# Kernel tuning notes

Hardware: AMD Instinct MI355X
Metric: run time of the kernel (lower is better)

Reference implementation:

```python
import math
import jax, jax.numpy as jnp
import numpy as np

L, F, K = 3, 128, 20          # layers, hidden size, rbf size
CUTOFF = 5.0
B, NPER, EPER = 4, 4096, 49152  # graphs, nodes/graph, edges/graph
NVOC = 119                    # len(ase.data.atomic_numbers)
PNAMES = ['atom_emb','pot_W','pot_b','init_W1','init_b1','init_W2','init_b2','vec_w',
          'filt_W','filt_b','msg_W1','msg_b1','msg_W2','msg_b2','U_W','V_W',
          'upd_W1','upd_b1','upd_W2','upd_b2']


def _painn(atom_xyz, cell, nodes, atom_edges, edges_displacement, V_flat, E_flat, p):
    N = B * NPER
    pos = atom_xyz.reshape(N, 3)
    # edge_offset = cumsum(num_nodes) ; all graphs have NPER nodes
    off = (jnp.arange(B, dtype=atom_edges.dtype) * NPER)[:, None, None]
    edges = (atom_edges + off).reshape(B * EPER, 2)
    # calc_distance with periodic cell offsets
    disp = jnp.einsum('bec,bcd->bed', edges_displacement, cell).reshape(B * EPER, 3)
    send, recv = edges[:, 0], edges[:, 1]
    diff = pos[recv] - (pos[send] + disp)                       # [E,3]
    dist = jnp.sqrt(jnp.sum(diff * diff, axis=1, keepdims=True))  # [E,1]
    # sinc RBF expansion
    n_range = jnp.arange(1, K + 1, dtype=jnp.float32)
    edge_state = jnp.sin(dist * n_range * (math.pi / CUTOFF)) / dist  # [E,K]
    # init scalar features: Embedding(Z) || Linear(V) -> MLP
    s_atom = p['atom_emb'][nodes.reshape(N)]                    # [N,F]
    s_pot = V_flat @ p['pot_W'].T + p['pot_b']                  # [N,F]
    h = jnp.concatenate([s_atom, s_pot], axis=-1)
    s = jax.nn.silu(h @ p['init_W1'].T + p['init_b1']) @ p['init_W2'].T + p['init_b2']  # [N,F]
    # init vector features: no-bias Linear(1->F) on E field
    v = E_flat[:, :, None] * p['vec_w']                         # [N,3,F]
    cut = jnp.where(dist < CUTOFF, 0.5 * (jnp.cos(math.pi * dist / CUTOFF) + 1.0), 0.0)  # [E,1]
    dirn = diff / jnp.maximum(dist, 1e-12)                      # [E,3]
    s_list, v_list = [], []
    for l in range(L):
        # --- PaiNNInteraction ---
        fw = (edge_state @ p['filt_W'][l].T + p['filt_b'][l]) * cut                # [E,3F]
        so = jax.nn.silu(s @ p['msg_W1'][l].T + p['msg_b1'][l]) @ p['msg_W2'][l].T + p['msg_b2'][l]  # [N,3F]
        fo = fw * so[send]                                                          # [E,3F]
        g_sv, g_ev, g_ns = jnp.split(fo, 3, axis=1)
        msg_s = s[send] * g_ns                                                      # [E,F]
        msg_v = v[send] * g_sv[:, None, :] + g_ev[:, None, :] * dirn[:, :, None]    # [E,3,F]
        s = s + jax.ops.segment_sum(msg_s, recv, num_segments=N)
        v = v + jax.ops.segment_sum(msg_v, recv, num_segments=N)
        # --- PaiNNUpdate ---
        Uv = v @ p['U_W'][l].T                                                      # [N,3,F]
        Vv = v @ p['V_W'][l].T                                                      # [N,3,F]
        Vn = jnp.sqrt(jnp.sum(Vv * Vv, axis=1))                                     # [N,F]
        m = jnp.concatenate([s, Vn], axis=1)
        m = jax.nn.silu(m @ p['upd_W1'][l].T + p['upd_b1'][l]) @ p['upd_W2'][l].T + p['upd_b2'][l]
        a_ss, a_sv, a_vv = jnp.split(m, 3, axis=1)
        s = s + a_ss + a_sv * jnp.sum(Uv * Vv, axis=1)
        v = v + a_vv[:, None, :] * Uv
        s_list.append(s)
        v_list.append(v)
    # pack trajectory: [L,N,1,F] scalar || [L,N,3,F] vector -> [L,N,4,F]
    return jnp.concatenate([jnp.stack(s_list)[:, :, None, :], jnp.stack(v_list)], axis=2)


def setup_inputs() -> dict:
    key = jax.random.key(0)
    ks = iter(jax.random.split(key, 48))
    def nrm(shape, scale=0.05):
        return jax.random.normal(next(ks), shape, dtype=jnp.float32) * scale
    atom_xyz = jax.random.uniform(next(ks), (B, NPER, 3), dtype=jnp.float32) * 30.0
    cell = jnp.tile(jnp.eye(3, dtype=jnp.float32)[None] * 30.0, (B, 1, 1))
    nodes = jax.random.randint(next(ks), (B, NPER), 0, NVOC)
    e0 = jax.random.randint(next(ks), (B, EPER), 0, NPER)
    delta = jax.random.randint(next(ks), (B, EPER), 1, NPER)
    e1 = (e0 + delta) % NPER  # sender != receiver -> no zero-distance edges
    atom_edges = jnp.stack([e0, e1], axis=-1)
    edges_displacement = jax.random.randint(next(ks), (B, EPER, 3), -1, 2).astype(jnp.float32)
    V_flat = nrm((B * NPER, 1), 1.0)
    E_flat = nrm((B * NPER, 3), 1.0)
    params = dict(
        atom_emb=nrm((NVOC, F), 1.0),
        pot_W=nrm((F, 1)), pot_b=nrm((F,)),
        init_W1=nrm((F, 2 * F)), init_b1=nrm((F,)),
        init_W2=nrm((F, F)), init_b2=nrm((F,)),
        vec_w=nrm((F,)),
        filt_W=nrm((L, 3 * F, K)), filt_b=nrm((L, 3 * F)),
        msg_W1=nrm((L, F, F)), msg_b1=nrm((L, F)),
        msg_W2=nrm((L, 3 * F, F)), msg_b2=nrm((L, 3 * F)),
        U_W=nrm((L, F, F)), V_W=nrm((L, F, F)),
        upd_W1=nrm((L, F, 2 * F)), upd_b1=nrm((L, F)),
        upd_W2=nrm((L, 3 * F, F)), upd_b2=nrm((L, 3 * F)),
    )
    return dict(atom_xyz=atom_xyz, cell=cell, nodes=nodes, atom_edges=atom_edges,
                edges_displacement=edges_displacement, V_flat=V_flat, E_flat=E_flat, **params)


def reference(atom_xyz, cell, nodes, atom_edges, edges_displacement, V_flat, E_flat,
              atom_emb, pot_W, pot_b, init_W1, init_b1, init_W2, init_b2, vec_w,
              filt_W, filt_b, msg_W1, msg_b1, msg_W2, msg_b2, U_W, V_W,
              upd_W1, upd_b1, upd_W2, upd_b2):
    p = dict(zip(PNAMES, (atom_emb, pot_W, pot_b, init_W1, init_b1, init_W2, init_b2, vec_w,
                          filt_W, filt_b, msg_W1, msg_b1, msg_W2, msg_b2, U_W, V_W,
                          upd_W1, upd_b1, upd_W2, upd_b2)))
    return _painn(atom_xyz, cell, nodes, atom_edges, edges_displacement, V_flat, E_flat, p)
```

## Files before the change

### kernel.cpp

```cpp
#include <hip/hip_runtime.h>
#include <math.h>

#define NPER  4096
#define NTOT  16384
#define EPER  49152
#define ETOT  196608
#define FD    128
#define F3    384
#define KR    20
#define PI_F  3.14159265358979f

typedef unsigned short u16;
typedef __attribute__((ext_vector_type(8))) short s16x8;
typedef __attribute__((ext_vector_type(4))) float f32x4;
typedef _Float16 h16x2 __attribute__((ext_vector_type(2)));
typedef _Float16 h16x4 __attribute__((ext_vector_type(4)));
typedef _Float16 h16x8 __attribute__((ext_vector_type(8)));

#if defined(__has_builtin)
#if __has_builtin(__builtin_amdgcn_fdot2)
#define FDOT2(a,b,c) __builtin_amdgcn_fdot2((a),(b),(c),false)
#endif
#endif
#ifndef FDOT2
#define FDOT2(a,b,c) ((float)(a)[0]*(float)(b)[0] + (float)(a)[1]*(float)(b)[1] + (c))
#endif

__device__ __forceinline__ float silu_f(float x){ return x / (1.0f + __expf(-x)); }
__device__ __forceinline__ u16 f2b(float x){
    unsigned u = __float_as_uint(x);
    u = u + 0x7FFFu + ((u >> 16) & 1u);
    return (u16)(u >> 16);
}
__device__ __forceinline__ float b2f(u16 h){ return __uint_as_float(((unsigned)h) << 16); }

struct __align__(16) EdgeRec {
    float4 ed;
    h16x8  es0;
    h16x8  es1;
    h16x4  es2;
    h16x4  pad;
};

__global__ __launch_bounds__(256) void edge_kernel(
    const float* __restrict__ xyz, const float* __restrict__ cell,
    const int* __restrict__ aedges, const float* __restrict__ edisp,
    int* __restrict__ sendb, int* __restrict__ recvb,
    EdgeRec* __restrict__ erec, int* __restrict__ counts)
{
    int e = blockIdx.x * blockDim.x + threadIdx.x;
    if (e >= ETOT) return;
    int b = e / EPER;
    int s = aedges[(size_t)e*2+0] + b*NPER;
    int r = aedges[(size_t)e*2+1] + b*NPER;
    const float* cb = cell + b*9;
    float c0 = edisp[(size_t)e*3+0], c1 = edisp[(size_t)e*3+1], c2 = edisp[(size_t)e*3+2];
    float diff[3];
    #pragma unroll
    for (int d=0; d<3; ++d) {
        float disp = c0*cb[d] + c1*cb[3+d] + c2*cb[6+d];
        diff[d] = xyz[(size_t)r*3+d] - (xyz[(size_t)s*3+d] + disp);
    }
    float dist = sqrtf(diff[0]*diff[0]+diff[1]*diff[1]+diff[2]*diff[2]);
    float cut = (dist < 5.0f) ? 0.5f*(__cosf(PI_F*dist*0.2f)+1.0f) : 0.0f;
    float invg = 1.0f/fmaxf(dist,1e-12f);
    EdgeRec rec;
    rec.ed = make_float4(diff[0]*invg, diff[1]*invg, diff[2]*invg, cut);
    float theta = dist*(PI_F*0.2f);
    float s1 = __sinf(theta), cth = __cosf(theta);
    float scale = cut / dist;
    float twoc = 2.f*cth;
    float sm1 = 0.f, sk = s1;
    _Float16 esv[20];
    #pragma unroll
    for (int k=0;k<20;++k){
        esv[k] = (_Float16)(sk*scale);
        float nx = twoc*sk - sm1;
        sm1 = sk; sk = nx;
    }
    union { h16x8 v; _Float16 h[8]; } u0, u1;
    union { h16x4 v; _Float16 h[4]; } u2;
    #pragma unroll
    for (int i=0;i<8;++i){ u0.h[i]=esv[i]; u1.h[i]=esv[8+i]; }
    #pragma unroll
    for (int i=0;i<4;++i) u2.h[i]=esv[16+i];
    rec.es0=u0.v; rec.es1=u1.v; rec.es2=u2.v;
    rec.pad = (h16x4)((_Float16)0);
    erec[e] = rec;
    sendb[e]=s; recvb[e]=r;
    atomicAdd(&counts[r],1);
}

__global__ __launch_bounds__(1024) void scan_kernel(const int* __restrict__ counts,
                                                    int* __restrict__ row_off)
{
    __shared__ int sdata[1024];
    int t = threadIdx.x;
    int base = t * 16;
    int local[16];
    int s = 0;
    #pragma unroll
    for (int i=0;i<16;++i){ local[i]=s; s += counts[base+i]; }
    sdata[t] = s;
    __syncthreads();
    for (int off=1; off<1024; off<<=1) {
        int val = (t>=off) ? sdata[t-off] : 0;
        __syncthreads();
        sdata[t] += val;
        __syncthreads();
    }
    int chunk_off = (t==0) ? 0 : sdata[t-1];
    #pragma unroll
    for (int i=0;i<16;++i) row_off[base+i] = chunk_off + local[i];
    if (t==1023) row_off[NTOT] = sdata[1023];
}

__global__ __launch_bounds__(256) void fill_kernel(
    const int* __restrict__ recvb, const int* __restrict__ sendb,
    const EdgeRec* __restrict__ erec,
    const int* __restrict__ row_off, int* __restrict__ cursor,
    int* __restrict__ sd_csr, EdgeRec* __restrict__ erec_csr)
{
    int e = blockIdx.x * blockDim.x + threadIdx.x;
    if (e >= ETOT) return;
    int r = recvb[e];
    int slot = atomicAdd(&cursor[r], 1);
    int pos = row_off[r] + slot;
    sd_csr[pos] = sendb[e];
    erec_csr[pos] = erec[e];
}

__global__ __launch_bounds__(256) void wconv_kernel(
    const float* __restrict__ w0, const float* __restrict__ w1,
    const float* __restrict__ w2, const float* __restrict__ w3,
    const float* __restrict__ w4, const float* __restrict__ w5,
    const float* __restrict__ w6, const float* __restrict__ w7,
    u16* __restrict__ dst)
{
    int t = blockIdx.x*256 + threadIdx.x;
    if (t >= 589824) return;
    const float* src; int off; int d = t;
    if      (t < 32768)  { src=w0; off=t; }
    else if (t < 49152)  { src=w1; off=t-32768; }
    else if (t < 98304)  { src=w2; off=t-49152; }
    else if (t < 245760) { src=w3; off=t-98304; }
    else if (t < 294912) { int o=t-245760; int l=o>>14; int r=o&16383; src=w4; off=o;
                           d = 245760 + l*32768 + r; }
    else if (t < 344064) { int o=t-294912; int l=o>>14; int r=o&16383; src=w5; off=o;
                           d = 245760 + l*32768 + 16384 + r; }
    else if (t < 442368) { src=w6; off=t-344064; }
    else                 { src=w7; off=t-442368; }
    dst[d] = f2b(src[off]);
}

__global__ __launch_bounds__(256) void wfilt_kernel(const float* __restrict__ fW,
                                                    _Float16* __restrict__ dst)
{
    int t = blockIdx.x*256 + threadIdx.x;
    if (t < 3*F3*KR) dst[t] = (_Float16)fW[t];
}

__global__ __launch_bounds__(256) void hbuild_kernel(const int* __restrict__ nodes,
    const float* __restrict__ atom_emb, const float* __restrict__ V_flat,
    const float* __restrict__ pot_W, const float* __restrict__ pot_b,
    u16* __restrict__ h)
{
    int t = blockIdx.x * blockDim.x + threadIdx.x;
    int n = t >> 8, k = t & 255;
    float val;
    if (k < FD) val = atom_emb[(size_t)nodes[n]*FD + k];
    else { int f = k - FD; val = V_flat[n]*pot_W[f] + pot_b[f]; }
    h[t] = f2b(val);
}

__global__ __launch_bounds__(256) void v0_kernel(const float* __restrict__ E_flat,
    const float* __restrict__ vec_w, float* __restrict__ v0, u16* __restrict__ vq)
{
    int t = blockIdx.x * blockDim.x + threadIdx.x;
    int n = t / F3, r = t - n*F3;
    int c = r >> 7, f = r & 127;
    float val = E_flat[(size_t)n*3 + c] * vec_w[f];
    v0[t] = val;
    vq[((size_t)n*FD + f)*4 + c] = f2b(val);
}

template<int ACT>
__global__ __launch_bounds__(256) void bgemm_kernel(
    const u16* __restrict__ A, int lda,
    const u16* __restrict__ W, int Kdim,
    const float* __restrict__ bias,
    float* __restrict__ C, int ldc,
    u16* __restrict__ Cb, int ldcb,
    u16* __restrict__ Cq, int qoff)
{
    const int tid  = threadIdx.x;
    const int wave = tid >> 6, lane = tid & 63;
    const int q = lane >> 4, im = lane & 15;
    const int row0 = blockIdx.y*64 + wave*16;
    const int col0 = blockIdx.x*64;
    f32x4 acc[4];
    #pragma unroll
    for (int n=0;n<4;++n) acc[n] = (f32x4){0.f,0.f,0.f,0.f};
    const u16* Ap = A + (size_t)(row0+im)*lda + q*8;
    const u16* Wp = W + (size_t)(col0+im)*Kdim + q*8;
    for (int k0 = 0; k0 < Kdim; k0 += 32) {
        s16x8 af = *(const s16x8*)(Ap + k0);
        #pragma unroll
        for (int n=0;n<4;++n) {
            s16x8 bf = *(const s16x8*)(Wp + (size_t)n*16*Kdim + k0);
            acc[n] = __builtin_amdgcn_mfma_f32_16x16x32_bf16(af, bf, acc[n], 0, 0, 0);
        }
    }
    #pragma unroll
    for (int n=0;n<4;++n) {
        int col = col0 + n*16 + im;
        float bv = bias ? bias[col] : 0.f;
        #pragma unroll
        for (int r=0;r<4;++r) {
            int row = row0 + q*4 + r;
            float v = acc[n][r] + bv;
            if (ACT) v = silu_f(v);
            if (C)  C[(size_t)row*ldc + col] = v;
            if (Cb) Cb[(size_t)row*ldcb + col] = f2b(v);
            if (Cq) Cq[((size_t)row*FD + (col & 127))*4 + (col >> 7) + qoff] = f2b(v);
        }
    }
}

#define HID_OFF(row, col2b) ((unsigned)((row)*256 + (col2b)*2) ^ ((unsigned)((row)&7) << 4))

__global__ __launch_bounds__(256) void msgmlp_kernel(
    const u16* __restrict__ A,
    const u16* __restrict__ W1,
    const float* __restrict__ b1,
    const u16* __restrict__ W2,
    const float* __restrict__ b2,
    u16* __restrict__ sq)
{
    __shared__ u16 hid[16*FD];
    const int tid = threadIdx.x;
    const int wave = tid >> 6, lane = tid & 63;
    const int q = lane >> 4, im = lane & 15;
    const int row0 = blockIdx.x * 16;
    {
        f32x4 acc[2];
        #pragma unroll
        for (int n=0;n<2;++n) acc[n] = (f32x4){0.f,0.f,0.f,0.f};
        const u16* Ap = A + (size_t)(row0+im)*FD + q*8;
        #pragma unroll
        for (int k0=0;k0<FD;k0+=32) {
            s16x8 af = *(const s16x8*)(Ap + k0);
            #pragma unroll
            for (int n=0;n<2;++n) {
                s16x8 bf = *(const s16x8*)(W1 + (size_t)(wave*32+n*16+im)*FD + k0 + q*8);
                acc[n] = __builtin_amdgcn_mfma_f32_16x16x32_bf16(af, bf, acc[n], 0, 0, 0);
            }
        }
        #pragma unroll
        for (int n=0;n<2;++n) {
            int col = wave*32 + n*16 + im;
            float bv = b1[col];
            #pragma unroll
            for (int r=0;r<4;++r) {
                int row = q*4 + r;
                *(u16*)((char*)hid + HID_OFF(row, col)) = f2b(silu_f(acc[n][r]+bv));
            }
        }
    }
    __syncthreads();
    s16x8 af[4];
    #pragma unroll
    for (int k=0;k<4;++k)
        af[k] = *(const s16x8*)((char*)hid + HID_OFF(im, k*32+q*8));
    #pragma unroll
    for (int jj=0;jj<2;++jj) {
        int j = wave*2 + jj;
        f32x4 a2[3];
        #pragma unroll
        for (int g=0;g<3;++g) a2[g] = (f32x4){0.f,0.f,0.f,0.f};
        #pragma unroll
        for (int k=0;k<4;++k) {
            #pragma unroll
            for (int g=0;g<3;++g) {
                s16x8 bf = *(const s16x8*)(W2 + (size_t)(g*128 + j*16 + im)*FD + k*32 + q*8);
                a2[g] = __builtin_amdgcn_mfma_f32_16x16x32_bf16(af[k], bf, a2[g], 0, 0, 0);
            }
        }
        int fcol = j*16 + im;
        float c0 = b2[fcol], c1 = b2[FD+fcol], c2 = b2[2*FD+fcol];
        #pragma unroll
        for (int r=0;r<4;++r) {
            int row = row0 + q*4 + r;
            size_t t4 = ((size_t)row*FD + fcol)*4;
            unsigned pk = (unsigned)f2b(a2[0][r]+c0) | ((unsigned)f2b(a2[1][r]+c1) << 16);
            *(unsigned*)(sq + t4) = pk;
            sq[t4+2] = f2b(a2[2][r]+c2);
        }
    }
}

__global__ __launch_bounds__(256) void updmlp_kernel(
    const u16* __restrict__ A,
    const u16* __restrict__ W1,
    const float* __restrict__ b1,
    const u16* __restrict__ W2,
    const float* __restrict__ b2,
    const float* __restrict__ s_mid, const float* __restrict__ dotb,
    const float* __restrict__ v_mid, const float* __restrict__ Uv,
    float* __restrict__ outp, u16* __restrict__ s_bf,
    u16* __restrict__ sq, u16* __restrict__ vq)
{
    __shared__ u16 hid[16*FD];
    const int tid = threadIdx.x;
    const int wave = tid >> 6, lane = tid & 63;
    const int q = lane >> 4, im = lane & 15;
    const int row0 = blockIdx.x * 16;
    {
        f32x4 acc[2];
        #pragma unroll
        for (int n=0;n<2;++n) acc[n] = (f32x4){0.f,0.f,0.f,0.f};
        const u16* Ap = A + (size_t)(row0+im)*256 + q*8;
        #pragma unroll
        for (int k0=0;k0<256;k0+=32) {
            s16x8 af = *(const s16x8*)(Ap + k0);
            #pragma unroll
            for (int n=0;n<2;++n) {
                s16x8 bf = *(const s16x8*)(W1 + (size_t)(wave*32+n*16+im)*256 + k0 + q*8);
                acc[n] = __builtin_amdgcn_mfma_f32_16x16x32_bf16(af, bf, acc[n], 0, 0, 0);
            }
        }
        #pragma unroll
        for (int n=0;n<2;++n) {
            int col = wave*32 + n*16 + im;
            float bv = b1[col];
            #pragma unroll
            for (int r=0;r<4;++r) {
                int row = q*4 + r;
                *(u16*)((char*)hid + HID_OFF(row, col)) = f2b(silu_f(acc[n][r]+bv));
            }
        }
    }
    __syncthreads();
    s16x8 af[4];
    #pragma unroll
    for (int k=0;k<4;++k)
        af[k] = *(const s16x8*)((char*)hid + HID_OFF(im, k*32+q*8));
    #pragma unroll
    for (int jj=0;jj<2;++jj) {
        int j = wave*2 + jj;
        f32x4 a2[3];
        #pragma unroll
        for (int g=0;g<3;++g) a2[g] = (f32x4){0.f,0.f,0.f,0.f};
        #pragma unroll
        for (int k=0;k<4;++k) {
            #pragma unroll
            for (int g=0;g<3;++g) {
                s16x8 bf = *(const s16x8*)(W2 + (size_t)(g*128 + j*16 + im)*FD + k*32 + q*8);
                a2[g] = __builtin_amdgcn_mfma_f32_16x16x32_bf16(af[k], bf, a2[g], 0, 0, 0);
            }
        }
        int fcol = j*16 + im;
        float b_ss = b2[fcol], b_sv = b2[FD+fcol], b_vv = b2[2*FD+fcol];
        #pragma unroll
        for (int r=0;r<4;++r) {
            int row = row0 + q*4 + r;
            float a_ss = a2[0][r] + b_ss;
            float a_sv = a2[1][r] + b_sv;
            float a_vv = a2[2][r] + b_vv;
            size_t t = (size_t)row*FD + fcol;
            float sval = s_mid[t] + a_ss + a_sv*dotb[t];
            outp[(size_t)row*512 + fcol] = sval;
            s_bf[t] = f2b(sval);
            sq[t*4 + 3] = f2b(sval);
            ushort4 pack;
            #pragma unroll
            for (int c=0;c<3;++c) {
                size_t vi = ((size_t)row*3 + c)*FD + fcol;
                float vval = v_mid[vi] + a_vv*Uv[((size_t)row*4 + c)*FD + fcol];
                outp[(size_t)row*512 + (1+c)*FD + fcol] = vval;
                ((u16*)&pack)[c] = f2b(vval);
            }
            ((u16*)&pack)[3] = 0;
            *(ushort4*)(vq + t*4) = pack;
        }
    }
}

__global__ __launch_bounds__(256) void uvdot_kernel(
    const u16* __restrict__ A,
    const u16* __restrict__ W,
    float* __restrict__ Uv,
    float* __restrict__ dotb,
    u16* __restrict__ mbuf)
{
    const int tid  = threadIdx.x;
    const int wave = tid >> 6, lane = tid & 63;
    const int q = lane >> 4, im = lane & 15;
    const int row0 = blockIdx.x*64 + wave*16;
    const int node = (row0 >> 2) + q;
    const u16* Ap = A + (size_t)(row0+im)*FD + q*8;
    s16x8 af[4];
    #pragma unroll
    for (int k=0;k<4;++k) af[k] = *(const s16x8*)(Ap + k*32);
    #pragma unroll
    for (int j=0;j<8;++j) {
        f32x4 aU = (f32x4){0.f,0.f,0.f,0.f};
        f32x4 aV = (f32x4){0.f,0.f,0.f,0.f};
        const u16* WpU = W + (size_t)(j*16+im)*FD + q*8;
        const u16* WpV = WpU + (size_t)128*FD;
        #pragma unroll
        for (int k=0;k<4;++k) {
            s16x8 bU = *(const s16x8*)(WpU + k*32);
            s16x8 bV = *(const s16x8*)(WpV + k*32);
            aU = __builtin_amdgcn_mfma_f32_16x16x32_bf16(af[k], bU, aU, 0, 0, 0);
            aV = __builtin_amdgcn_mfma_f32_16x16x32_bf16(af[k], bV, aV, 0, 0, 0);
        }
        int fcol = j*16 + im;
        float u0=aU[0], u1=aU[1], u2=aU[2];
        float w0=aV[0], w1=aV[1], w2=aV[2];
        dotb[(size_t)node*FD + fcol] = u0*w0 + u1*w1 + u2*w2;
        mbuf[(size_t)node*256 + FD + fcol] = f2b(sqrtf(w0*w0 + w1*w1 + w2*w2));
        size_t ub = ((size_t)node*4)*FD + fcol;
        Uv[ub]      = u0;
        Uv[ub+FD]   = u1;
        Uv[ub+2*FD] = u2;
    }
}

__device__ __forceinline__ void edge_step(
    const EdgeRec& er, ushort4 s4, ushort4 v4,
    const h16x2* wp,
    float b0, float b1, float b2,
    float& acc_s, float& av0, float& av1, float& av2)
{
    union { h16x8 v; h16x2 p[4]; } e0, e1;
    union { h16x4 v; h16x2 p[2]; } e2;
    e0.v = er.es0; e1.v = er.es1; e2.v = er.es2;
    h16x2 ep[10] = {e0.p[0],e0.p[1],e0.p[2],e0.p[3],
                    e1.p[0],e1.p[1],e1.p[2],e1.p[3],
                    e2.p[0],e2.p[1]};
    float4 ed = er.ed;
    float d0=0.f, d1=0.f, d2=0.f;
    #pragma unroll
    for (int j=0;j<10;++j){
        d0 = FDOT2(ep[j], wp[j],    d0);
        d1 = FDOT2(ep[j], wp[10+j], d1);
        d2 = FDOT2(ep[j], wp[20+j], d2);
    }
    float g_sv = d0 + b0*ed.w;
    float g_ev = d1 + b1*ed.w;
    float g_ns = d2 + b2*ed.w;
    float fo_sv = g_sv * b2f(s4.x);
    float fo_ev = g_ev * b2f(s4.y);
    float fo_ns = g_ns * b2f(s4.z);
    acc_s += b2f(s4.w) * fo_ns;
    av0 += b2f(v4.x)*fo_sv + fo_ev*ed.x;
    av1 += b2f(v4.y)*fo_sv + fo_ev*ed.y;
    av2 += b2f(v4.z)*fo_sv + fo_ev*ed.z;
}

__global__ __launch_bounds__(256) __attribute__((amdgpu_waves_per_eu(4,8)))
void agg_kernel(
    const float* __restrict__ s_prev_f, int s_ldaf,
    const float* __restrict__ v_prev_f, int v_nstrf,
    const ushort4* __restrict__ sq, const ushort4* __restrict__ vq,
    const EdgeRec* __restrict__ erec_csr,
    const int* __restrict__ sd_csr, const int* __restrict__ row_off,
    const _Float16* __restrict__ wf, const float* __restrict__ fb,
    float* __restrict__ s_mid, float* __restrict__ v_mid,
    u16* __restrict__ vmid4_bf, u16* __restrict__ mbuf)
{
    const int f   = threadIdx.x & 127;
    const int sub = threadIdx.x >> 7;
    h16x2 wp[30];
    #pragma unroll
    for (int rsel=0; rsel<3; ++rsel){
        const h16x4* rp = (const h16x4*)(wf + (size_t)(rsel*FD + f)*KR);
        #pragma unroll
        for (int i=0;i<5;++i){
            union { h16x4 v; h16x2 p[2]; } t; t.v = rp[i];
            wp[rsel*10+2*i]   = t.p[0];
            wp[rsel*10+2*i+1] = t.p[1];
        }
    }
    const float b0 = fb[f], b1 = fb[FD+f], b2 = fb[2*FD+f];

    const int n = blockIdx.x*2 + sub;
    const int beg = __builtin_amdgcn_readfirstlane(row_off[n]);
    const int end = __builtin_amdgcn_readfirstlane(row_off[n+1]);
    float acc_s=0.f, av0=0.f, av1=0.f, av2=0.f;

    int i0 = (beg   < end) ? beg   : 0;
    int i1 = (beg+1 < end) ? beg+1 : i0;
    int sd0 = __builtin_amdgcn_readfirstlane(sd_csr[i0]);
    int sd1 = __builtin_amdgcn_readfirstlane(sd_csr[i1]);
    ushort4 sA = sq[(size_t)sd0*FD + f];
    ushort4 vA = vq[(size_t)sd0*FD + f];
    ushort4 sB = sq[(size_t)sd1*FD + f];
    ushort4 vB = vq[(size_t)sd1*FD + f];
    EdgeRec r0 = erec_csr[i0];
    EdgeRec r1 = erec_csr[i1];

    for (int idx = beg; idx + 2 <= end; idx += 2) {
        int j0 = (idx+2 < end) ? idx+2 : 0;
        int j1 = (idx+3 < end) ? idx+3 : j0;
        int nsd0 = __builtin_amdgcn_readfirstlane(sd_csr[j0]);
        int nsd1 = __builtin_amdgcn_readfirstlane(sd_csr[j1]);
        ushort4 nsA = sq[(size_t)nsd0*FD + f];
        ushort4 nvA = vq[(size_t)nsd0*FD + f];
        ushort4 nsB = sq[(size_t)nsd1*FD + f];
        ushort4 nvB = vq[(size_t)nsd1*FD + f];
        EdgeRec nr0 = erec_csr[j0];
        EdgeRec nr1 = erec_csr[j1];

        edge_step(r0, sA, vA, wp, b0,b1,b2, acc_s, av0, av1, av2);
        edge_step(r1, sB, vB, wp, b0,b1,b2, acc_s, av0, av1, av2);

        sA=nsA; vA=nvA; sB=nsB; vB=nvB; r0=nr0; r1=nr1;
    }
    if (((end - beg) & 1) && beg < end) {
        edge_step(r0, sA, vA, wp, b0,b1,b2, acc_s, av0, av1, av2);
    }

    float smv = s_prev_f[(size_t)n*s_ldaf+f] + acc_s;
    s_mid[(size_t)n*FD+f] = smv;
    mbuf[(size_t)n*256+f] = f2b(smv);
    const float* vp = v_prev_f + (size_t)n*v_nstrf;
    float o0 = vp[f]+av0, o1 = vp[FD+f]+av1, o2 = vp[2*FD+f]+av2;
    size_t vo = (size_t)n*F3;
    v_mid[vo+f]=o0;        v_mid[vo+FD+f]=o1;        v_mid[vo+2*FD+f]=o2;
    size_t v4 = (size_t)n*512;
    vmid4_bf[v4+f]=f2b(o0); vmid4_bf[v4+FD+f]=f2b(o1); vmid4_bf[v4+2*FD+f]=f2b(o2);
}

extern "C" void kernel_launch(void* const* d_in, const int* in_sizes, int n_in,
                              void* d_out, int out_size, void* d_ws, size_t ws_size,
                              hipStream_t stream)
{
    (void)in_sizes; (void)n_in; (void)out_size; (void)ws_size;
    const float* atom_xyz = (const float*)d_in[0];
    const float* cell     = (const float*)d_in[1];
    const int*   nodes    = (const int*)d_in[2];
    const int*   aedges   = (const int*)d_in[3];
    const float* edisp    = (const float*)d_in[4];
    const float* V_flat   = (const float*)d_in[5];
    const float* E_flat   = (const float*)d_in[6];
    const float* atom_emb = (const float*)d_in[7];
    const float* pot_W    = (const float*)d_in[8];
    const float* pot_b    = (const float*)d_in[9];
    const float* init_W1  = (const float*)d_in[10];
    const float* init_b1  = (const float*)d_in[11];
    const float* init_W2  = (const float*)d_in[12];
    const float* init_b2  = (const float*)d_in[13];
    const float* vec_w    = (const float*)d_in[14];
    const float* filt_W   = (const float*)d_in[15];
    const float* filt_b   = (const float*)d_in[16];
    const float* msg_W1   = (const float*)d_in[17];
    const float* msg_b1   = (const float*)d_in[18];
    const float* msg_W2   = (const float*)d_in[19];
    const float* msg_b2   = (const float*)d_in[20];
    const float* U_W      = (const float*)d_in[21];
    const float* V_W      = (const float*)d_in[22];
    const float* upd_W1   = (const float*)d_in[23];
    const float* upd_b1   = (const float*)d_in[24];
    const float* upd_W2   = (const float*)d_in[25];
    const float* upd_b2   = (const float*)d_in[26];

    float* out = (float*)d_out;
    char* base = (char*)d_ws;
    size_t o = 0;
    auto alloc = [&](size_t bytes)->char* { char* r = base + o; o += (bytes + 255) & ~(size_t)255; return r; };

    float* s0     = (float*)alloc((size_t)NTOT*FD*4);
    float* v0     = (float*)alloc((size_t)NTOT*F3*4);
    float* s_mid  = (float*)alloc((size_t)NTOT*FD*4);
    float* v_mid  = (float*)alloc((size_t)NTOT*F3*4);
    float* Uv4    = (float*)alloc((size_t)NTOT*4*FD*4);
    float* dotb   = (float*)alloc((size_t)NTOT*FD*4);
    EdgeRec* erec     = (EdgeRec*)alloc((size_t)ETOT*sizeof(EdgeRec));
    EdgeRec* erec_csr = (EdgeRec*)alloc((size_t)ETOT*sizeof(EdgeRec));
    u16* h_bf     = (u16*)alloc((size_t)NTOT*256*2);
    u16* s_bf     = (u16*)alloc((size_t)NTOT*FD*2);
    u16* sq       = (u16*)alloc((size_t)NTOT*FD*4*2);
    u16* vq       = (u16*)alloc((size_t)NTOT*FD*4*2);
    u16* hid_bf   = (u16*)alloc((size_t)NTOT*FD*2);
    u16* vmid4_bf = (u16*)alloc((size_t)NTOT*4*FD*2);
    u16* wts      = (u16*)alloc((size_t)589824*2);
    _Float16* wf16 = (_Float16*)alloc((size_t)3*F3*KR*2);
    int* sendb    = (int*)alloc((size_t)ETOT*4);
    int* recvb    = (int*)alloc((size_t)ETOT*4);
    int* sd_csr   = (int*)alloc((size_t)ETOT*4);
    int* row_off  = (int*)alloc((size_t)(NTOT+1)*4);
    int* counts   = (int*)alloc((size_t)NTOT*4);
    int* cursor   = (int*)alloc((size_t)NTOT*4);

    hipMemsetAsync(counts, 0, NTOT*sizeof(int), stream);
    hipMemsetAsync(cursor, 0, NTOT*sizeof(int), stream);
    hipMemsetAsync(vmid4_bf, 0, (size_t)NTOT*4*FD*2, stream);

    edge_kernel<<<ETOT/256, 256, 0, stream>>>(atom_xyz, cell, aedges, edisp,
        sendb, recvb, erec, counts);
    scan_kernel<<<1, 1024, 0, stream>>>(counts, row_off);
    fill_kernel<<<ETOT/256, 256, 0, stream>>>(recvb, sendb, erec,
        row_off, cursor, sd_csr, erec_csr);
    wconv_kernel<<<(589824+255)/256, 256, 0, stream>>>(
        init_W1, init_W2, msg_W1, msg_W2, U_W, V_W, upd_W1, upd_W2, wts);
    wfilt_kernel<<<(3*F3*KR+255)/256, 256, 0, stream>>>(filt_W, wf16);

    const u16* w_init1 = wts + 0;
    const u16* w_init2 = wts + 32768;
    const u16* w_msg1  = wts + 49152;
    const u16* w_msg2  = wts + 98304;
    const u16* w_UV    = wts + 245760;
    const u16* w_upd1  = wts + 344064;
    const u16* w_upd2  = wts + 442368;

    hbuild_kernel<<<NTOT*256/256, 256, 0, stream>>>(nodes, atom_emb, V_flat, pot_W, pot_b, h_bf);
    bgemm_kernel<1><<<dim3(FD/64, NTOT/64), 256, 0, stream>>>(
        h_bf, 256, w_init1, 256, init_b1, (float*)nullptr, 0, hid_bf, FD, (u16*)nullptr, 0);
    bgemm_kernel<0><<<dim3(FD/64, NTOT/64), 256, 0, stream>>>(
        hid_bf, FD, w_init2, FD, init_b2, s0, FD, s_bf, FD, sq, 3);
    v0_kernel<<<NTOT*F3/256, 256, 0, stream>>>(E_flat, vec_w, v0, vq);

    const float* s_prev_f = s0;  int s_ldaf  = FD;
    const float* v_prev_f = v0;  int v_nstrf = 3*FD;
    for (int l = 0; l < 3; ++l) {
        msgmlp_kernel<<<NTOT/16, 256, 0, stream>>>(
            s_bf, w_msg1 + (size_t)l*16384, msg_b1 + (size_t)l*FD,
            w_msg2 + (size_t)l*49152, msg_b2 + (size_t)l*F3, sq);
        agg_kernel<<<NTOT/2, 256, 0, stream>>>(s_prev_f, s_ldaf, v_prev_f, v_nstrf,
            (const ushort4*)sq, (const ushort4*)vq, erec_csr, sd_csr, row_off,
            wf16 + (size_t)l*F3*KR, filt_b + (size_t)l*F3, s_mid, v_mid, vmid4_bf, h_bf);
        uvdot_kernel<<<NTOT*4/64, 256, 0, stream>>>(
            vmid4_bf, w_UV + (size_t)l*32768, Uv4, dotb, h_bf);
        float* outp = out + (size_t)l*NTOT*512;
        updmlp_kernel<<<NTOT/16, 256, 0, stream>>>(
            h_bf, w_upd1 + (size_t)l*32768, upd_b1 + (size_t)l*FD,
            w_upd2 + (size_t)l*49152, upd_b2 + (size_t)l*F3,
            s_mid, dotb, v_mid, Uv4, outp, s_bf, sq, vq);
        s_prev_f = outp;        s_ldaf  = 512;
        v_prev_f = outp + FD;   v_nstrf = 512;
    }
}
```

Baseline: 711.5 us.

## Fuse U/V projection into update MLP and compute edge geometry in CSR fill

The uvdot kernel is merged into the update-MLP kernel. Uv, the dot product and the norm features now live in shared memory instead of global buffers, which removes the Uv4/dotb/h_bf round trips and one launch per layer. The edge preprocessing is also split: a light count kernel runs first, then the geometry and RBF work is done directly in the fill kernel, writing CSR order without the intermediate erec/sendb/recvb arrays. The cost is higher shared-memory use per block, which may lower occupancy, and s_mid is re-read and converted inside the fused kernel.

```diff
diff --git a/kernel.cpp b/kernel.cpp
--- a/kernel.cpp
+++ b/kernel.cpp
@@ -9,6 +9,7 @@
 #define F3    384
 #define KR    20
 #define PI_F  3.14159265358979f
+#define PADF  132
 
 typedef unsigned short u16;
 typedef __attribute__((ext_vector_type(8))) short s16x8;
@@ -42,11 +43,44 @@
     h16x4  pad;
 };
 
-__global__ __launch_bounds__(256) void edge_kernel(
+__global__ __launch_bounds__(256) void ecount_kernel(
+    const int* __restrict__ aedges, int* __restrict__ counts)
+{
+    int e = blockIdx.x * blockDim.x + threadIdx.x;
+    if (e >= ETOT) return;
+    int r = aedges[(size_t)e*2+1] + (e / EPER)*NPER;
+    atomicAdd(&counts[r],1);
+}
+
+__global__ __launch_bounds__(1024) void scan_kernel(const int* __restrict__ counts,
+                                                    int* __restrict__ row_off)
+{
+    __shared__ int sdata[1024];
+    int t = threadIdx.x;
+    int base = t * 16;
+    int local[16];
+    int s = 0;
+    #pragma unroll
+    for (int i=0;i<16;++i){ local[i]=s; s += counts[base+i]; }
+    sdata[t] = s;
+    __syncthreads();
+    for (int off=1; off<1024; off<<=1) {
+        int val = (t>=off) ? sdata[t-off] : 0;
+        __syncthreads();
+        sdata[t] += val;
+        __syncthreads();
+    }
+    int chunk_off = (t==0) ? 0 : sdata[t-1];
+    #pragma unroll
+    for (int i=0;i<16;++i) row_off[base+i] = chunk_off + local[i];
+    if (t==1023) row_off[NTOT] = sdata[1023];
+}
+
+__global__ __launch_bounds__(256) void fill_kernel(
     const float* __restrict__ xyz, const float* __restrict__ cell,
     const int* __restrict__ aedges, const float* __restrict__ edisp,
-    int* __restrict__ sendb, int* __restrict__ recvb,
-    EdgeRec* __restrict__ erec, int* __restrict__ counts)
+    const int* __restrict__ row_off, int* __restrict__ cursor,
+    int* __restrict__ sd_csr, EdgeRec* __restrict__ erec_csr)
 {
     int e = blockIdx.x * blockDim.x + threadIdx.x;
     if (e >= ETOT) return;
@@ -86,48 +120,10 @@
     for (int i=0;i<4;++i) u2.h[i]=esv[16+i];
     rec.es0=u0.v; rec.es1=u1.v; rec.es2=u2.v;
     rec.pad = (h16x4)((_Float16)0);
-    erec[e] = rec;
-    sendb[e]=s; recvb[e]=r;
-    atomicAdd(&counts[r],1);
-}
-
-__global__ __launch_bounds__(1024) void scan_kernel(const int* __restrict__ counts,
-                                                    int* __restrict__ row_off)
-{
-    __shared__ int sdata[1024];
-    int t = threadIdx.x;
-    int base = t * 16;
-    int local[16];
-    int s = 0;
-    #pragma unroll
-    for (int i=0;i<16;++i){ local[i]=s; s += counts[base+i]; }
-    sdata[t] = s;
-    __syncthreads();
-    for (int off=1; off<1024; off<<=1) {
-        int val = (t>=off) ? sdata[t-off] : 0;
-        __syncthreads();
-        sdata[t] += val;
-        __syncthreads();
-    }
-    int chunk_off = (t==0) ? 0 : sdata[t-1];
-    #pragma unroll
-    for (int i=0;i<16;++i) row_off[base+i] = chunk_off + local[i];
-    if (t==1023) row_off[NTOT] = sdata[1023];
-}
-
-__global__ __launch_bounds__(256) void fill_kernel(
-    const int* __restrict__ recvb, const int* __restrict__ sendb,
-    const EdgeRec* __restrict__ erec,
-    const int* __restrict__ row_off, int* __restrict__ cursor,
-    int* __restrict__ sd_csr, EdgeRec* __restrict__ erec_csr)
-{
-    int e = blockIdx.x * blockDim.x + threadIdx.x;
-    if (e >= ETOT) return;
-    int r = recvb[e];
     int slot = atomicAdd(&cursor[r], 1);
     int pos = row_off[r] + slot;
-    sd_csr[pos] = sendb[e];
-    erec_csr[pos] = erec[e];
+    sd_csr[pos] = s;
+    erec_csr[pos] = rec;
 }
 
 __global__ __launch_bounds__(256) void wconv_kernel(
@@ -228,6 +224,7 @@
 }
 
 #define HID_OFF(row, col2b) ((unsigned)((row)*256 + (col2b)*2) ^ ((unsigned)((row)&7) << 4))
+#define M_OFF(row, col2b)   ((unsigned)((row)*512 + (col2b)*2) ^ ((unsigned)((row)&7) << 4))
 
 __global__ __launch_bounds__(256) void msgmlp_kernel(
     const u16* __restrict__ A,
@@ -299,30 +296,73 @@
     }
 }
 
-__global__ __launch_bounds__(256) void updmlp_kernel(
-    const u16* __restrict__ A,
+__global__ __launch_bounds__(256) void upduv_kernel(
+    const u16* __restrict__ vmid4,
+    const u16* __restrict__ Wuv,
     const u16* __restrict__ W1,
     const float* __restrict__ b1,
     const u16* __restrict__ W2,
     const float* __restrict__ b2,
-    const float* __restrict__ s_mid, const float* __restrict__ dotb,
-    const float* __restrict__ v_mid, const float* __restrict__ Uv,
+    const float* __restrict__ s_mid, const float* __restrict__ v_mid,
     float* __restrict__ outp, u16* __restrict__ s_bf,
     u16* __restrict__ sq, u16* __restrict__ vq)
 {
-    __shared__ u16 hid[16*FD];
+    __shared__ u16   mL[16*256];
+    __shared__ float dotL[16*PADF];
+    __shared__ float uvL[48*PADF];
+    __shared__ u16   hid[16*FD];
     const int tid = threadIdx.x;
     const int wave = tid >> 6, lane = tid & 63;
     const int q = lane >> 4, im = lane & 15;
-    const int row0 = blockIdx.x * 16;
+    const int node0 = blockIdx.x * 16;
+
+    {
+        const int prow0 = blockIdx.x*64 + wave*16;
+        const u16* Ap = vmid4 + (size_t)(prow0+im)*FD + q*8;
+        s16x8 af[4];
+        #pragma unroll
+        for (int k=0;k<4;++k) af[k] = *(const s16x8*)(Ap + k*32);
+        const int nloc = wave*4 + q;
+        #pragma unroll
+        for (int j=0;j<8;++j) {
+            f32x4 aU = (f32x4){0.f,0.f,0.f,0.f};
+            f32x4 aV = (f32x4){0.f,0.f,0.f,0.f};
+            const u16* WpU = Wuv + (size_t)(j*16+im)*FD + q*8;
+            const u16* WpV = WpU + (size_t)128*FD;
+            #pragma unroll
+            for (int k=0;k<4;++k) {
+                s16x8 bU = *(const s16x8*)(WpU + k*32);
+                s16x8 bV = *(const s16x8*)(WpV + k*32);
+                aU = __builtin_amdgcn_mfma_f32_16x16x32_bf16(af[k], bU, aU, 0, 0, 0);
+                aV = __builtin_amdgcn_mfma_f32_16x16x32_bf16(af[k], bV, aV, 0, 0, 0);
+            }
+            int fcol = j*16 + im;
+            float u0=aU[0], u1=aU[1], u2=aU[2];
+            float w0=aV[0], w1=aV[1], w2=aV[2];
+            dotL[nloc*PADF + fcol] = u0*w0 + u1*w1 + u2*w2;
+            *(u16*)((char*)mL + M_OFF(nloc, 128+fcol)) = f2b(sqrtf(w0*w0+w1*w1+w2*w2));
+            uvL[(nloc*3+0)*PADF + fcol] = u0;
+            uvL[(nloc*3+1)*PADF + fcol] = u1;
+            uvL[(nloc*3+2)*PADF + fcol] = u2;
+        }
+    }
+    {
+        int row = tid >> 4;
+        int c0  = (tid & 15) * 8;
+        const float* sp = s_mid + (size_t)(node0+row)*FD + c0;
+        union { s16x8 v; u16 h[8]; } pk;
+        #pragma unroll
+        for (int i=0;i<8;++i) pk.h[i] = f2b(sp[i]);
+        *(s16x8*)((char*)mL + M_OFF(row, c0)) = pk.v;
+    }
+    __syncthreads();
     {
         f32x4 acc[2];
         #pragma unroll
         for (int n=0;n<2;++n) acc[n] = (f32x4){0.f,0.f,0.f,0.f};
-        const u16* Ap = A + (size_t)(row0+im)*256 + q*8;
         #pragma unroll
         for (int k0=0;k0<256;k0+=32) {
-            s16x8 af = *(const s16x8*)(Ap + k0);
+            s16x8 af = *(const s16x8*)((char*)mL + M_OFF(im, k0+q*8));
             #pragma unroll
             for (int n=0;n<2;++n) {
                 s16x8 bf = *(const s16x8*)(W1 + (size_t)(wave*32+n*16+im)*256 + k0 + q*8);
@@ -341,10 +381,10 @@
         }
     }
     __syncthreads();
-    s16x8 af[4];
+    s16x8 af2[4];
     #pragma unroll
     for (int k=0;k<4;++k)
-        af[k] = *(const s16x8*)((char*)hid + HID_OFF(im, k*32+q*8));
+        af2[k] = *(const s16x8*)((char*)hid + HID_OFF(im, k*32+q*8));
     #pragma unroll
     for (int jj=0;jj<2;++jj) {
         int j = wave*2 + jj;
@@ -356,19 +396,20 @@
             #pragma unroll
             for (int g=0;g<3;++g) {
                 s16x8 bf = *(const s16x8*)(W2 + (size_t)(g*128 + j*16 + im)*FD + k*32 + q*8);
-                a2[g] = __builtin_amdgcn_mfma_f32_16x16x32_bf16(af[k], bf, a2[g], 0, 0, 0);
+                a2[g] = __builtin_amdgcn_mfma_f32_16x16x32_bf16(af2[k], bf, a2[g], 0, 0, 0);
             }
         }
         int fcol = j*16 + im;
         float b_ss = b2[fcol], b_sv = b2[FD+fcol], b_vv = b2[2*FD+fcol];
         #pragma unroll
         for (int r=0;r<4;++r) {
-            int row = row0 + q*4 + r;
+            int rl = q*4 + r;
+            int row = node0 + rl;
             float a_ss = a2[0][r] + b_ss;
             float a_sv = a2[1][r] + b_sv;
             float a_vv = a2[2][r] + b_vv;
             size_t t = (size_t)row*FD + fcol;
-            float sval = s_mid[t] + a_ss + a_sv*dotb[t];
+            float sval = s_mid[t] + a_ss + a_sv*dotL[rl*PADF + fcol];
             outp[(size_t)row*512 + fcol] = sval;
             s_bf[t] = f2b(sval);
             sq[t*4 + 3] = f2b(sval);
@@ -376,54 +417,13 @@
             #pragma unroll
             for (int c=0;c<3;++c) {
                 size_t vi = ((size_t)row*3 + c)*FD + fcol;
-                float vval = v_mid[vi] + a_vv*Uv[((size_t)row*4 + c)*FD + fcol];
+                float vval = v_mid[vi] + a_vv*uvL[(rl*3+c)*PADF + fcol];
                 outp[(size_t)row*512 + (1+c)*FD + fcol] = vval;
                 ((u16*)&pack)[c] = f2b(vval);
             }
             ((u16*)&pack)[3] = 0;
             *(ushort4*)(vq + t*4) = pack;
         }
-    }
-}
-
-__global__ __launch_bounds__(256) void uvdot_kernel(
-    const u16* __restrict__ A,
-    const u16* __restrict__ W,
-    float* __restrict__ Uv,
-    float* __restrict__ dotb,
-    u16* __restrict__ mbuf)
-{
-    const int tid  = threadIdx.x;
-    const int wave = tid >> 6, lane = tid & 63;
-    const int q = lane >> 4, im = lane & 15;
-    const int row0 = blockIdx.x*64 + wave*16;
-    const int node = (row0 >> 2) + q;
-    const u16* Ap = A + (size_t)(row0+im)*FD + q*8;
-    s16x8 af[4];
-    #pragma unroll
-    for (int k=0;k<4;++k) af[k] = *(const s16x8*)(Ap + k*32);
-    #pragma unroll
-    for (int j=0;j<8;++j) {
-        f32x4 aU = (f32x4){0.f,0.f,0.f,0.f};
-        f32x4 aV = (f32x4){0.f,0.f,0.f,0.f};
-        const u16* WpU = W + (size_t)(j*16+im)*FD + q*8;
-        const u16* WpV = WpU + (size_t)128*FD;
-        #pragma unroll
-        for (int k=0;k<4;++k) {
-            s16x8 bU = *(const s16x8*)(WpU + k*32);
-            s16x8 bV = *(const s16x8*)(WpV + k*32);
-            aU = __builtin_amdgcn_mfma_f32_16x16x32_bf16(af[k], bU, aU, 0, 0, 0);
-            aV = __builtin_amdgcn_mfma_f32_16x16x32_bf16(af[k], bV, aV, 0, 0, 0);
-        }
-        int fcol = j*16 + im;
-        float u0=aU[0], u1=aU[1], u2=aU[2];
-        float w0=aV[0], w1=aV[1], w2=aV[2];
-        dotb[(size_t)node*FD + fcol] = u0*w0 + u1*w1 + u2*w2;
-        mbuf[(size_t)node*256 + FD + fcol] = f2b(sqrtf(w0*w0 + w1*w1 + w2*w2));
-        size_t ub = ((size_t)node*4)*FD + fcol;
-        Uv[ub]      = u0;
-        Uv[ub+FD]   = u1;
-        Uv[ub+2*FD] = u2;
     }
 }
 
@@ -468,7 +468,7 @@
     const int* __restrict__ sd_csr, const int* __restrict__ row_off,
     const _Float16* __restrict__ wf, const float* __restrict__ fb,
     float* __restrict__ s_mid, float* __restrict__ v_mid,
-    u16* __restrict__ vmid4_bf, u16* __restrict__ mbuf)
+    u16* __restrict__ vmid4_bf)
 {
     const int f   = threadIdx.x & 127;
     const int sub = threadIdx.x >> 7;
@@ -524,7 +524,6 @@
 
     float smv = s_prev_f[(size_t)n*s_ldaf+f] + acc_s;
     s_mid[(size_t)n*FD+f] = smv;
-    mbuf[(size_t)n*256+f] = f2b(smv);
     const float* vp = v_prev_f + (size_t)n*v_nstrf;
     float o0 = vp[f]+av0, o1 = vp[FD+f]+av1, o2 = vp[2*FD+f]+av2;
     size_t vo = (size_t)n*F3;
@@ -575,9 +574,6 @@
     float* v0     = (float*)alloc((size_t)NTOT*F3*4);
     float* s_mid  = (float*)alloc((size_t)NTOT*FD*4);
     float* v_mid  = (float*)alloc((size_t)NTOT*F3*4);
-    float* Uv4    = (float*)alloc((size_t)NTOT*4*FD*4);
-    float* dotb   = (float*)alloc((size_t)NTOT*FD*4);
-    EdgeRec* erec     = (EdgeRec*)alloc((size_t)ETOT*sizeof(EdgeRec));
     EdgeRec* erec_csr = (EdgeRec*)alloc((size_t)ETOT*sizeof(EdgeRec));
     u16* h_bf     = (u16*)alloc((size_t)NTOT*256*2);
     u16* s_bf     = (u16*)alloc((size_t)NTOT*FD*2);
@@ -587,8 +583,6 @@
     u16* vmid4_bf = (u16*)alloc((size_t)NTOT*4*FD*2);
     u16* wts      = (u16*)alloc((size_t)589824*2);
     _Float16* wf16 = (_Float16*)alloc((size_t)3*F3*KR*2);
-    int* sendb    = (int*)alloc((size_t)ETOT*4);
-    int* recvb    = (int*)alloc((size_t)ETOT*4);
     int* sd_csr   = (int*)alloc((size_t)ETOT*4);
     int* row_off  = (int*)alloc((size_t)(NTOT+1)*4);
     int* counts   = (int*)alloc((size_t)NTOT*4);
@@ -598,10 +592,9 @@
     hipMemsetAsync(cursor, 0, NTOT*sizeof(int), stream);
     hipMemsetAsync(vmid4_bf, 0, (size_t)NTOT*4*FD*2, stream);
 
-    edge_kernel<<<ETOT/256, 256, 0, stream>>>(atom_xyz, cell, aedges, edisp,
-        sendb, recvb, erec, counts);
+    ecount_kernel<<<ETOT/256, 256, 0, stream>>>(aedges, counts);
     scan_kernel<<<1, 1024, 0, stream>>>(counts, row_off);
-    fill_kernel<<<ETOT/256, 256, 0, stream>>>(recvb, sendb, erec,
+    fill_kernel<<<ETOT/256, 256, 0, stream>>>(atom_xyz, cell, aedges, edisp,
         row_off, cursor, sd_csr, erec_csr);
     wconv_kernel<<<(589824+255)/256, 256, 0, stream>>>(
         init_W1, init_W2, msg_W1, msg_W2, U_W, V_W, upd_W1, upd_W2, wts);
@@ -630,14 +623,13 @@
             w_msg2 + (size_t)l*49152, msg_b2 + (size_t)l*F3, sq);
         agg_kernel<<<NTOT/2, 256, 0, stream>>>(s_prev_f, s_ldaf, v_prev_f, v_nstrf,
             (const ushort4*)sq, (const ushort4*)vq, erec_csr, sd_csr, row_off,
-            wf16 + (size_t)l*F3*KR, filt_b + (size_t)l*F3, s_mid, v_mid, vmid4_bf, h_bf);
-        uvdot_kernel<<<NTOT*4/64, 256, 0, stream>>>(
-            vmid4_bf, w_UV + (size_t)l*32768, Uv4, dotb, h_bf);
+            wf16 + (size_t)l*F3*KR, filt_b + (size_t)l*F3, s_mid, v_mid, vmid4_bf);
         float* outp = out + (size_t)l*NTOT*512;
-        updmlp_kernel<<<NTOT/16, 256, 0, stream>>>(
-            h_bf, w_upd1 + (size_t)l*32768, upd_b1 + (size_t)l*FD,
+        upduv_kernel<<<NTOT/16, 256, 0, stream>>>(
+            vmid4_bf, w_UV + (size_t)l*32768,
+            w_upd1 + (size_t)l*32768, upd_b1 + (size_t)l*FD,
             w_upd2 + (size_t)l*49152, upd_b2 + (size_t)l*F3,
-            s_mid, dotb, v_mid, Uv4, outp, s_bf, sq, vq);
+            s_mid, v_mid, outp, s_bf, sq, vq);
         s_prev_f = outp;        s_ldaf  = 512;
         v_prev_f = outp + FD;   v_nstrf = 512;
     }
```

New measurement: 658.4 us. 1.08x faster.
